# Kernel tuning notes

Hardware: AMD Instinct MI355X
Metric: run time of the kernel (lower is better)

Reference implementation:

```python
import jax, jax.numpy as jnp
import numpy as np

D_MODEL = 1024
NUM_HEADS = 16
D_K = D_MODEL // NUM_HEADS


def setup_inputs() -> dict:
    key = jax.random.key(0)
    ks = jax.random.split(key, 5)
    s = 1.0 / np.sqrt(D_MODEL)
    return {
        "x": jax.random.normal(ks[0], (2, 2048, D_MODEL), dtype=jnp.float32),
        "Wq": jax.random.normal(ks[1], (D_MODEL, D_MODEL), dtype=jnp.float32) * s,
        "bq": jnp.zeros((D_MODEL,), jnp.float32),
        "Wk": jax.random.normal(ks[2], (D_MODEL, D_MODEL), dtype=jnp.float32) * s,
        "bk": jnp.zeros((D_MODEL,), jnp.float32),
        "Wv": jax.random.normal(ks[3], (D_MODEL, D_MODEL), dtype=jnp.float32) * s,
        "bv": jnp.zeros((D_MODEL,), jnp.float32),
        "Wo": jax.random.normal(ks[4], (D_MODEL, D_MODEL), dtype=jnp.float32) * s,
        "bo": jnp.zeros((D_MODEL,), jnp.float32),
    }


def reference(x, Wq, bq, Wk, bk, Wv, bv, Wo, bo):
    B, S, _ = x.shape

    def split_heads(t):  # [B,S,D] -> [B,H,S,d_k]
        return t.reshape(B, S, NUM_HEADS, D_K).transpose(0, 2, 1, 3)

    q = split_heads(x @ Wq + bq)
    k = split_heads(x @ Wk + bk)
    v = split_heads(x @ Wv + bv)

    # [B,H,S,S] scores, scaled by 1/sqrt(d_k)
    scores = jnp.einsum("bhqd,bhkd->bhqk", q, k) / jnp.sqrt(jnp.float32(D_K))
    causal = jnp.tril(jnp.ones((S, S), dtype=bool))  # True = keep
    scores = jnp.where(causal, scores, -jnp.inf)
    attn = jax.nn.softmax(scores, axis=-1)
    # dropout is identity in eval mode
    out = jnp.einsum("bhqk,bhkd->bhqd", attn, v)
    out = out.transpose(0, 2, 1, 3).reshape(B, S, D_MODEL)
    return out @ Wo + bo
```

## Files before the change

### kernel.cpp

```cpp
#include <hip/hip_runtime.h>
#include <stdint.h>

typedef __attribute__((ext_vector_type(8))) short bf16x8;
typedef __attribute__((ext_vector_type(8))) unsigned short ushort8;
typedef __attribute__((ext_vector_type(4))) float f32x4;
typedef __attribute__((ext_vector_type(16))) float f32x16;

constexpr int DM = 1024;
constexpr int SQ = 2048;
constexpr int NB = 2;
constexpr int NH = 16;
constexpr int DK = 64;
constexpr int M  = NB * SQ;

__device__ inline float bf2f(unsigned short u) {
    union { uint32_t i; float f; } c; c.i = ((uint32_t)u) << 16; return c.f;
}
__device__ inline unsigned short f2bf(float f) {
    union { float f; uint32_t i; } c; c.f = f;
    uint32_t r = c.i + 0x7FFFu + ((c.i >> 16) & 1u);
    return (unsigned short)(r >> 16);
}
__device__ inline uint32_t cvtpk(float lo, float hi) {
    uint32_t r;
    asm("v_cvt_pk_bf16_f32 %0, %1, %2" : "=v"(r) : "v"(lo), "v"(hi));
    return r;
}
__device__ inline uint32_t sx32(uint32_t v) {
    return (uint32_t)__shfl_xor((int)v, 32);
}
__device__ inline bf16x8 mkfrag(uint32_t a, uint32_t b, uint32_t c, uint32_t d) {
    union { bf16x8 v; uint32_t u[4]; } m;
    m.u[0] = a; m.u[1] = b; m.u[2] = c; m.u[3] = d;
    return m.v;
}
__device__ inline void gload_lds16(const unsigned short* g, unsigned short* l) {
    __builtin_amdgcn_global_load_lds(
        (const __attribute__((address_space(1))) void*)g,
        (__attribute__((address_space(3))) void*)l, 16, 0, 0);
}

__global__ __launch_bounds__(256) void cvt_x(const float* __restrict__ x,
                                             unsigned short* __restrict__ xb) {
    int idx = (blockIdx.x * 256 + threadIdx.x) * 8;
    const float* p = x + idx;
    ushort8 o;
#pragma unroll
    for (int i = 0; i < 8; ++i) o[i] = f2bf(p[i]);
    *(ushort8*)(xb + idx) = o;
}

__global__ __launch_bounds__(256) void cvt_w(const float* __restrict__ W,
                                             unsigned short* __restrict__ Wt) {
    __shared__ float tile[32][33];
    int tx = threadIdx.x, ty = threadIdx.y;
    int bx = blockIdx.x, by = blockIdx.y;
#pragma unroll
    for (int j = 0; j < 4; ++j)
        tile[ty + j * 8][tx] = W[(size_t)(by * 32 + ty + j * 8) * DM + bx * 32 + tx];
    __syncthreads();
#pragma unroll
    for (int j = 0; j < 4; ++j)
        Wt[(size_t)(bx * 32 + ty + j * 8) * DM + by * 32 + tx] = f2bf(tile[tx][ty + j * 8]);
}

template <int MODE>
__global__ __launch_bounds__(256) void gemm128(const unsigned short* __restrict__ A,
                                               const unsigned short* __restrict__ Bt,
                                               const float* __restrict__ b0,
                                               const float* __restrict__ b1,
                                               const float* __restrict__ b2,
                                               void* __restrict__ outp) {
    constexpr int K = 1024;
    __shared__ __align__(16) unsigned short As[128 * 32];
    __shared__ __align__(16) unsigned short Bs[128 * 32];
    const int t = threadIdx.x;
    const int w = t >> 6, l = t & 63;
    const int l15 = l & 15, lg = l >> 4;
    const int wr = w >> 1, wc = w & 1;
    const int bx = blockIdx.x, by = blockIdx.y;

    f32x4 acc[4][4] = {};

    const int srow = l >> 2;
    const int sk   = (l & 3) * 8;
    const unsigned short* Abase = A  + (size_t)(by * 128) * K;
    const unsigned short* Bbase = Bt + (size_t)(bx * 128) * K;

    for (int k0 = 0; k0 < K; k0 += 32) {
#pragma unroll
        for (int i = 0; i < 2; ++i) {
            const int row = w * 32 + i * 16 + srow;
            gload_lds16(Abase + (size_t)row * K + k0 + sk, &As[row * 32 + sk]);
            gload_lds16(Bbase + (size_t)row * K + k0 + sk, &Bs[row * 32 + sk]);
        }
        __syncthreads();

        bf16x8 af[4], bfr[4];
#pragma unroll
        for (int mi = 0; mi < 4; ++mi)
            af[mi] = *(const bf16x8*)&As[(wr * 64 + mi * 16 + l15) * 32 + lg * 8];
#pragma unroll
        for (int ni = 0; ni < 4; ++ni)
            bfr[ni] = *(const bf16x8*)&Bs[(wc * 64 + ni * 16 + l15) * 32 + lg * 8];
#pragma unroll
        for (int mi = 0; mi < 4; ++mi)
#pragma unroll
            for (int ni = 0; ni < 4; ++ni)
                acc[mi][ni] = __builtin_amdgcn_mfma_f32_16x16x32_bf16(af[mi], bfr[ni], acc[mi][ni], 0, 0, 0);
        __syncthreads();
    }

#pragma unroll
    for (int ni = 0; ni < 4; ++ni) {
        const int n = bx * 128 + wc * 64 + ni * 16 + l15;
        float bias;
        if constexpr (MODE == 0) {
            const int mat = n >> 10;
            const float* bp = (mat == 0) ? b0 : (mat == 1) ? b1 : b2;
            bias = bp[n & 1023];
        } else {
            bias = b0[n];
        }
#pragma unroll
        for (int mi = 0; mi < 4; ++mi)
#pragma unroll
            for (int i = 0; i < 4; ++i) {
                const int m = by * 128 + wr * 64 + mi * 16 + lg * 4 + i;
                const float v = acc[mi][ni][i] + bias;
                if constexpr (MODE == 0) {
                    const int mat = n >> 10, c = n & 1023;
                    const int h = c >> 6, d = c & 63;
                    const int b = m >> 11, si = m & 2047;
                    size_t idx;
                    if (mat == 2)
                        idx = ((size_t)(b * NH + h) * DK + d) * SQ + si;
                    else
                        idx = ((size_t)(b * NH + h) * SQ + si) * DK + d;
                    ((unsigned short*)outp)[(size_t)mat * (NB * NH * SQ * DK) + idx] = f2bf(v);
                } else {
                    ((float*)outp)[(size_t)m * DM + n] = v;
                }
            }
    }
}

__global__ __launch_bounds__(128) void attn32(const unsigned short* __restrict__ Qg,
                                              const unsigned short* __restrict__ Kg,
                                              const unsigned short* __restrict__ Vtg,
                                              unsigned short* __restrict__ O) {
    __shared__ __align__(16) char Ks0[8192];
    __shared__ __align__(16) char Vs0[8192];
    __shared__ __align__(16) char Ks1[8192];
    __shared__ __align__(16) char Vs1[8192];
    const float NEG_INF = -__builtin_inff();

    const int bid = blockIdx.x;
    const int bh  = bid & 31;
    const int g   = bid >> 5;
    const int u = g & 7, sq = g >> 3;
    const int qt_even = 2 * u + (sq >> 1);
    const int qt_odd  = 31 - 2 * u - (sq >> 1);
    const int qt = (sq & 1) ? qt_odd : qt_even;

    const int b = bh >> 4, h = bh & 15;
    const size_t base = (size_t)bh * SQ * DK;

    const int t = threadIdx.x;
    const int w = t >> 6, l = t & 63;
    const int l31 = l & 31, hi = l >> 5;
    const bool h0 = (hi == 0);

    const int lrow = l >> 3;
    const int lchunk = (l & 7) ^ lrow;
    const unsigned short* ksrc0 = Kg + base + (size_t)lrow * DK + lchunk * 8;
    const unsigned short* vsrc0 = Vtg + (size_t)(bh * 64 + lrow) * SQ + lchunk * 8;

    int roff[4];
#pragma unroll
    for (int c = 0; c < 4; ++c) roff[c] = (hi * 16 + 32 * c) ^ ((l & 7) << 4);
    const int rb0 = l31 * 128, rb1 = (32 + l31) * 128;

    const int qrow = qt * 64 + w * 32 + l31;
    const int qloc = w * 32 + l31;

    bf16x8 qf[4];
    {
        const unsigned short* qp = Qg + base + (size_t)qrow * DK + hi * 8;
#pragma unroll
        for (int c = 0; c < 4; ++c) qf[c] = *(const bf16x8*)(qp + 16 * c);
    }

    float mrun = NEG_INF, lsum = 0.f;
    f32x16 o0 = {}, o1 = {};

    auto STAGE = [&](int kt, unsigned short* Kd, unsigned short* Vd) {
        if (w == 0) {
            const unsigned short* ks = ksrc0 + (size_t)kt * 64 * DK;
#pragma unroll
            for (int i = 0; i < 8; ++i)
                gload_lds16(ks + i * 8 * DK, Kd + i * 512 + l * 8);
        } else {
            const unsigned short* vs = vsrc0 + kt * 64;
#pragma unroll
            for (int i = 0; i < 8; ++i)
                gload_lds16(vs + (size_t)i * 8 * SQ, Vd + i * 512 + l * 8);
        }
    };

    auto COMPUTE = [&](int kt, const char* KB, const char* VB) {
        f32x16 s0 = {}, s1 = {};
#pragma unroll
        for (int c = 0; c < 4; ++c) {
            bf16x8 ka0 = *(const bf16x8*)(KB + rb0 + roff[c]);
            bf16x8 ka1 = *(const bf16x8*)(KB + rb1 + roff[c]);
            s0 = __builtin_amdgcn_mfma_f32_32x32x16_bf16(ka0, qf[c], s0, 0, 0, 0);
            s1 = __builtin_amdgcn_mfma_f32_32x32x16_bf16(ka1, qf[c], s1, 0, 0, 0);
        }

        const bool diag = (kt == qt);
        float p[32];
        float tm = NEG_INF;
#pragma unroll
        for (int r = 0; r < 16; ++r) {
            const int key0 = (r & 3) + 8 * (r >> 2) + 4 * hi;
            float v0 = s0[r] * 0.125f;
            float v1 = s1[r] * 0.125f;
            if (diag && key0 > qloc) v0 = NEG_INF;
            if (diag && key0 + 32 > qloc) v1 = NEG_INF;
            p[r] = v0; p[16 + r] = v1;
            tm = fmaxf(tm, fmaxf(v0, v1));
        }
        tm = fmaxf(tm, __shfl_xor(tm, 32));
        const float mn = fmaxf(mrun, tm);
        const float corr = __expf(mrun - mn);
        mrun = mn;
        float ps = 0.f;
#pragma unroll
        for (int r = 0; r < 32; ++r) { p[r] = __expf(p[r] - mn); ps += p[r]; }
        lsum = lsum * corr + ps;
#pragma unroll
        for (int r = 0; r < 16; ++r) { o0[r] *= corr; o1[r] *= corr; }

        uint32_t pk[16];
#pragma unroll
        for (int i = 0; i < 16; ++i) pk[i] = cvtpk(p[2 * i], p[2 * i + 1]);
        const uint32_t X1 = sx32(h0 ? pk[2]  : pk[0]);
        const uint32_t X2 = sx32(h0 ? pk[3]  : pk[1]);
        const uint32_t X3 = sx32(h0 ? pk[6]  : pk[4]);
        const uint32_t X4 = sx32(h0 ? pk[7]  : pk[5]);
        const uint32_t X5 = sx32(h0 ? pk[10] : pk[8]);
        const uint32_t X6 = sx32(h0 ? pk[11] : pk[9]);
        const uint32_t X7 = sx32(h0 ? pk[14] : pk[12]);
        const uint32_t X8 = sx32(h0 ? pk[15] : pk[13]);
        bf16x8 pf[4];
        pf[0] = mkfrag(h0 ? pk[0]  : X1, h0 ? pk[1]  : X2, h0 ? X1 : pk[2],  h0 ? X2 : pk[3]);
        pf[1] = mkfrag(h0 ? pk[4]  : X3, h0 ? pk[5]  : X4, h0 ? X3 : pk[6],  h0 ? X4 : pk[7]);
        pf[2] = mkfrag(h0 ? pk[8]  : X5, h0 ? pk[9]  : X6, h0 ? X5 : pk[10], h0 ? X6 : pk[11]);
        pf[3] = mkfrag(h0 ? pk[12] : X7, h0 ? pk[13] : X8, h0 ? X7 : pk[14], h0 ? X8 : pk[15]);

#pragma unroll
        for (int s = 0; s < 4; ++s) {
            bf16x8 va0 = *(const bf16x8*)(VB + rb0 + roff[s]);
            bf16x8 va1 = *(const bf16x8*)(VB + rb1 + roff[s]);
            o0 = __builtin_amdgcn_mfma_f32_32x32x16_bf16(va0, pf[s], o0, 0, 0, 0);
            o1 = __builtin_amdgcn_mfma_f32_32x32x16_bf16(va1, pf[s], o1, 0, 0, 0);
        }
    };

    STAGE(0, (unsigned short*)Ks0, (unsigned short*)Vs0);
    __syncthreads();

#pragma unroll 1
    for (int kt = 0; kt <= qt; kt += 2) {
        if (kt + 1 <= qt) STAGE(kt + 1, (unsigned short*)Ks1, (unsigned short*)Vs1);
        COMPUTE(kt, Ks0, Vs0);
        __syncthreads();
        if (kt + 1 > qt) break;
        if (kt + 2 <= qt) STAGE(kt + 2, (unsigned short*)Ks0, (unsigned short*)Vs0);
        COMPUTE(kt + 1, Ks1, Vs1);
        __syncthreads();
    }

    lsum += __shfl_xor(lsum, 32);
    const float inv = 1.f / lsum;
    unsigned short* op = O + ((size_t)(b * SQ + qrow)) * DM + h * 64;
#pragma unroll
    for (int r = 0; r < 16; r += 2) {
        const int d = (r & 3) + 8 * (r >> 2) + 4 * hi;
        uint32_t w0 = (uint32_t)f2bf(o0[r] * inv) | ((uint32_t)f2bf(o0[r + 1] * inv) << 16);
        uint32_t w1 = (uint32_t)f2bf(o1[r] * inv) | ((uint32_t)f2bf(o1[r + 1] * inv) << 16);
        *(uint32_t*)(op + d) = w0;
        *(uint32_t*)(op + 32 + d) = w1;
    }
}

extern "C" void kernel_launch(void* const* d_in, const int* in_sizes, int n_in,
                              void* d_out, int out_size, void* d_ws, size_t ws_size,
                              hipStream_t stream) {
    const float* x  = (const float*)d_in[0];
    const float* Wq = (const float*)d_in[1];
    const float* bq = (const float*)d_in[2];
    const float* Wk = (const float*)d_in[3];
    const float* bk = (const float*)d_in[4];
    const float* Wv = (const float*)d_in[5];
    const float* bv = (const float*)d_in[6];
    const float* Wo = (const float*)d_in[7];
    const float* bo = (const float*)d_in[8];
    float* out = (float*)d_out;

    char* ws = (char*)d_ws;
    const size_t XB_BYTES = (size_t)M * DM * 2;
    const size_t W_BYTES  = (size_t)DM * DM * 2;
    const size_t H_BYTES  = (size_t)NB * NH * SQ * DK * 2;
    unsigned short* xb  = (unsigned short*)ws;
    unsigned short* wqt = (unsigned short*)(ws + XB_BYTES);
    unsigned short* wkt = (unsigned short*)(ws + XB_BYTES + W_BYTES);
    unsigned short* wvt = (unsigned short*)(ws + XB_BYTES + 2 * W_BYTES);
    unsigned short* wot = (unsigned short*)(ws + XB_BYTES + 3 * W_BYTES);
    unsigned short* Qb  = (unsigned short*)(ws + XB_BYTES + 4 * W_BYTES);
    unsigned short* Kb  = (unsigned short*)(ws + XB_BYTES + 4 * W_BYTES + H_BYTES);
    unsigned short* Vb  = (unsigned short*)(ws + XB_BYTES + 4 * W_BYTES + 2 * H_BYTES);

    cvt_x<<<(M * DM) / (256 * 8), 256, 0, stream>>>(x, xb);
    dim3 wgrid(32, 32), wblk(32, 8);
    cvt_w<<<wgrid, wblk, 0, stream>>>(Wq, wqt);
    cvt_w<<<wgrid, wblk, 0, stream>>>(Wk, wkt);
    cvt_w<<<wgrid, wblk, 0, stream>>>(Wv, wvt);
    cvt_w<<<wgrid, wblk, 0, stream>>>(Wo, wot);

    gemm128<0><<<dim3(24, 32), 256, 0, stream>>>(xb, wqt, bq, bk, bv, Qb);

    attn32<<<NB * NH * 32, 128, 0, stream>>>(Qb, Kb, Vb, xb );

    gemm128<1><<<dim3(8, 32), 256, 0, stream>>>(xb, wot, bo, bo, bo, out);
}
```

Before: 135.7 us.

## Double-buffer projection GEMM, fold softmax scale into Q, lazy rescale with exp2

The projection GEMM now double-buffers its A/B LDS tiles so global loads for the next K-slice overlap MFMA work on the current one. The softmax scale and log2(e) are folded into Q at the projection epilogue, so attention can use the raw v_exp_f32 (exp2) instruction without a per-score multiply. Attention also skips the running-max rescale unless some lane's max grows by more than a threshold, uses tree reductions for max and sum, and raises wave priority around MFMA blocks. The price is more LDS in the GEMM and a softmax whose numerics depend on the rescale threshold, which bounds how far values can drift before rescaling.

```diff
diff --git a/kernel.cpp b/kernel.cpp
--- a/kernel.cpp
+++ b/kernel.cpp
@@ -20,6 +20,11 @@
     union { float f; uint32_t i; } c; c.f = f;
     uint32_t r = c.i + 0x7FFFu + ((c.i >> 16) & 1u);
     return (unsigned short)(r >> 16);
+}
+__device__ inline float exp2v(float x) {
+    float r;
+    asm("v_exp_f32 %0, %1" : "=v"(r) : "v"(x));
+    return r;
 }
 __device__ inline uint32_t cvtpk(float lo, float hi) {
     uint32_t r;
@@ -72,8 +77,10 @@
                                                const float* __restrict__ b2,
                                                void* __restrict__ outp) {
     constexpr int K = 1024;
-    __shared__ __align__(16) unsigned short As[128 * 32];
-    __shared__ __align__(16) unsigned short Bs[128 * 32];
+    __shared__ __align__(16) unsigned short As0[128 * 32];
+    __shared__ __align__(16) unsigned short Bs0[128 * 32];
+    __shared__ __align__(16) unsigned short As1[128 * 32];
+    __shared__ __align__(16) unsigned short Bs1[128 * 32];
     const int t = threadIdx.x;
     const int w = t >> 6, l = t & 63;
     const int l15 = l & 15, lg = l >> 4;
@@ -87,27 +94,38 @@
     const unsigned short* Abase = A  + (size_t)(by * 128) * K;
     const unsigned short* Bbase = Bt + (size_t)(bx * 128) * K;
 
-    for (int k0 = 0; k0 < K; k0 += 32) {
+    auto STAGE = [&](int k0, unsigned short* Ad, unsigned short* Bd) {
 #pragma unroll
         for (int i = 0; i < 2; ++i) {
             const int row = w * 32 + i * 16 + srow;
-            gload_lds16(Abase + (size_t)row * K + k0 + sk, &As[row * 32 + sk]);
-            gload_lds16(Bbase + (size_t)row * K + k0 + sk, &Bs[row * 32 + sk]);
-        }
-        __syncthreads();
-
+            gload_lds16(Abase + (size_t)row * K + k0 + sk, Ad + row * 32 + sk);
+            gload_lds16(Bbase + (size_t)row * K + k0 + sk, Bd + row * 32 + sk);
+        }
+    };
+    auto COMPUTE = [&](const unsigned short* Asb, const unsigned short* Bsb) {
         bf16x8 af[4], bfr[4];
 #pragma unroll
         for (int mi = 0; mi < 4; ++mi)
-            af[mi] = *(const bf16x8*)&As[(wr * 64 + mi * 16 + l15) * 32 + lg * 8];
+            af[mi] = *(const bf16x8*)&Asb[(wr * 64 + mi * 16 + l15) * 32 + lg * 8];
 #pragma unroll
         for (int ni = 0; ni < 4; ++ni)
-            bfr[ni] = *(const bf16x8*)&Bs[(wc * 64 + ni * 16 + l15) * 32 + lg * 8];
+            bfr[ni] = *(const bf16x8*)&Bsb[(wc * 64 + ni * 16 + l15) * 32 + lg * 8];
 #pragma unroll
         for (int mi = 0; mi < 4; ++mi)
 #pragma unroll
             for (int ni = 0; ni < 4; ++ni)
                 acc[mi][ni] = __builtin_amdgcn_mfma_f32_16x16x32_bf16(af[mi], bfr[ni], acc[mi][ni], 0, 0, 0);
+    };
+
+    STAGE(0, As0, Bs0);
+    __syncthreads();
+#pragma unroll 1
+    for (int k0 = 0; k0 < K; k0 += 64) {
+        if (k0 + 32 < K) STAGE(k0 + 32, As1, Bs1);
+        COMPUTE(As0, Bs0);
+        __syncthreads();
+        if (k0 + 64 < K) STAGE(k0 + 64, As0, Bs0);
+        COMPUTE(As1, Bs1);
         __syncthreads();
     }
 
@@ -127,9 +145,10 @@
 #pragma unroll
             for (int i = 0; i < 4; ++i) {
                 const int m = by * 128 + wr * 64 + mi * 16 + lg * 4 + i;
-                const float v = acc[mi][ni][i] + bias;
+                float v = acc[mi][ni][i] + bias;
                 if constexpr (MODE == 0) {
                     const int mat = n >> 10, c = n & 1023;
+                    if (mat == 0) v *= 0.18033688f;
                     const int h = c >> 6, d = c & 63;
                     const int b = m >> 11, si = m & 2047;
                     size_t idx;
@@ -158,10 +177,10 @@
     const int bid = blockIdx.x;
     const int bh  = bid & 31;
     const int g   = bid >> 5;
-    const int u = g & 7, sq = g >> 3;
-    const int qt_even = 2 * u + (sq >> 1);
-    const int qt_odd  = 31 - 2 * u - (sq >> 1);
-    const int qt = (sq & 1) ? qt_odd : qt_even;
+    const int u = g & 7, gq = g >> 3;
+    const int qt_even = 2 * u + (gq >> 1);
+    const int qt_odd  = 31 - 2 * u - (gq >> 1);
+    const int qt = (gq & 1) ? qt_odd : qt_even;
 
     const int b = bh >> 4, h = bh & 15;
     const size_t base = (size_t)bh * SQ * DK;
@@ -209,42 +228,57 @@
     };
 
     auto COMPUTE = [&](int kt, const char* KB, const char* VB) {
-        f32x16 s0 = {}, s1 = {};
+        f32x16 s0v = {}, s1v = {};
+        __builtin_amdgcn_s_setprio(1);
 #pragma unroll
         for (int c = 0; c < 4; ++c) {
             bf16x8 ka0 = *(const bf16x8*)(KB + rb0 + roff[c]);
             bf16x8 ka1 = *(const bf16x8*)(KB + rb1 + roff[c]);
-            s0 = __builtin_amdgcn_mfma_f32_32x32x16_bf16(ka0, qf[c], s0, 0, 0, 0);
-            s1 = __builtin_amdgcn_mfma_f32_32x32x16_bf16(ka1, qf[c], s1, 0, 0, 0);
-        }
-
-        const bool diag = (kt == qt);
-        float p[32];
-        float tm = NEG_INF;
-#pragma unroll
-        for (int r = 0; r < 16; ++r) {
-            const int key0 = (r & 3) + 8 * (r >> 2) + 4 * hi;
-            float v0 = s0[r] * 0.125f;
-            float v1 = s1[r] * 0.125f;
-            if (diag && key0 > qloc) v0 = NEG_INF;
-            if (diag && key0 + 32 > qloc) v1 = NEG_INF;
-            p[r] = v0; p[16 + r] = v1;
-            tm = fmaxf(tm, fmaxf(v0, v1));
-        }
+            s0v = __builtin_amdgcn_mfma_f32_32x32x16_bf16(ka0, qf[c], s0v, 0, 0, 0);
+            s1v = __builtin_amdgcn_mfma_f32_32x32x16_bf16(ka1, qf[c], s1v, 0, 0, 0);
+        }
+        __builtin_amdgcn_s_setprio(0);
+
+        float s[32];
+#pragma unroll
+        for (int r = 0; r < 16; ++r) { s[r] = s0v[r]; s[16 + r] = s1v[r]; }
+        if (kt == qt) {
+#pragma unroll
+            for (int r = 0; r < 16; ++r) {
+                const int key0 = (r & 3) + 8 * (r >> 2) + 4 * hi;
+                if (key0 > qloc) s[r] = NEG_INF;
+                if (key0 + 32 > qloc) s[16 + r] = NEG_INF;
+            }
+        }
+
+        float t8[8];
+#pragma unroll
+        for (int i = 0; i < 8; ++i)
+            t8[i] = fmaxf(fmaxf(s[i], s[i + 8]), fmaxf(s[i + 16], s[i + 24]));
+        float tm = fmaxf(fmaxf(fmaxf(t8[0], t8[1]), fmaxf(t8[2], t8[3])),
+                         fmaxf(fmaxf(t8[4], t8[5]), fmaxf(t8[6], t8[7])));
         tm = fmaxf(tm, __shfl_xor(tm, 32));
+
         const float mn = fmaxf(mrun, tm);
-        const float corr = __expf(mrun - mn);
-        mrun = mn;
-        float ps = 0.f;
-#pragma unroll
-        for (int r = 0; r < 32; ++r) { p[r] = __expf(p[r] - mn); ps += p[r]; }
-        lsum = lsum * corr + ps;
-#pragma unroll
-        for (int r = 0; r < 16; ++r) { o0[r] *= corr; o1[r] *= corr; }
+        if (!__all(tm - mrun <= 11.0f)) {
+            const float corr = exp2v(mrun - mn);
+            lsum *= corr;
+#pragma unroll
+            for (int r = 0; r < 16; ++r) { o0[r] *= corr; o1[r] *= corr; }
+            mrun = mn;
+        }
+
+#pragma unroll
+        for (int r = 0; r < 32; ++r) s[r] = exp2v(s[r] - mrun);
+        float a8[8];
+#pragma unroll
+        for (int i = 0; i < 8; ++i)
+            a8[i] = (s[i] + s[i + 8]) + (s[i + 16] + s[i + 24]);
+        lsum += ((a8[0] + a8[1]) + (a8[2] + a8[3])) + ((a8[4] + a8[5]) + (a8[6] + a8[7]));
 
         uint32_t pk[16];
 #pragma unroll
-        for (int i = 0; i < 16; ++i) pk[i] = cvtpk(p[2 * i], p[2 * i + 1]);
+        for (int i = 0; i < 16; ++i) pk[i] = cvtpk(s[2 * i], s[2 * i + 1]);
         const uint32_t X1 = sx32(h0 ? pk[2]  : pk[0]);
         const uint32_t X2 = sx32(h0 ? pk[3]  : pk[1]);
         const uint32_t X3 = sx32(h0 ? pk[6]  : pk[4]);
@@ -259,13 +293,15 @@
         pf[2] = mkfrag(h0 ? pk[8]  : X5, h0 ? pk[9]  : X6, h0 ? X5 : pk[10], h0 ? X6 : pk[11]);
         pf[3] = mkfrag(h0 ? pk[12] : X7, h0 ? pk[13] : X8, h0 ? X7 : pk[14], h0 ? X8 : pk[15]);
 
-#pragma unroll
-        for (int s = 0; s < 4; ++s) {
-            bf16x8 va0 = *(const bf16x8*)(VB + rb0 + roff[s]);
-            bf16x8 va1 = *(const bf16x8*)(VB + rb1 + roff[s]);
-            o0 = __builtin_amdgcn_mfma_f32_32x32x16_bf16(va0, pf[s], o0, 0, 0, 0);
-            o1 = __builtin_amdgcn_mfma_f32_32x32x16_bf16(va1, pf[s], o1, 0, 0, 0);
-        }
+        __builtin_amdgcn_s_setprio(1);
+#pragma unroll
+        for (int vi = 0; vi < 4; ++vi) {
+            bf16x8 va0 = *(const bf16x8*)(VB + rb0 + roff[vi]);
+            bf16x8 va1 = *(const bf16x8*)(VB + rb1 + roff[vi]);
+            o0 = __builtin_amdgcn_mfma_f32_32x32x16_bf16(va0, pf[vi], o0, 0, 0, 0);
+            o1 = __builtin_amdgcn_mfma_f32_32x32x16_bf16(va1, pf[vi], o1, 0, 0, 0);
+        }
+        __builtin_amdgcn_s_setprio(0);
     };
 
     STAGE(0, (unsigned short*)Ks0, (unsigned short*)Vs0);
```

Result: slower. 157.1 us (+15.8%).
